# Kernel optimization log

Hardware: AMD Instinct MI355X
Metric: run time of the kernel (lower is better)

The kernel has to match this reference:

```python
import jax, jax.numpy as jnp
import numpy as np

B, NCLASS, NSUPP = 4096, 1000, 64
NCHUNK = NSUPP * NSUPP  # 4096, x's feature dim


def setup_inputs() -> dict:
    key = jax.random.key(0)
    k1, k2, k3 = jax.random.split(key, 3)
    x = jax.random.normal(k1, (B, NCHUNK), dtype=jnp.float32)
    # torch .uniform_(-1, 1)
    wSupp = jax.random.uniform(k2, (NCLASS, NSUPP), dtype=jnp.float32, minval=-1.0, maxval=1.0)
    chunk_map = jax.random.randint(k3, (NCLASS, NSUPP), 0, NCHUNK, dtype=jnp.int32)
    return {"x": x, "wSupp": wSupp, "chunk_map": chunk_map}


def reference(x, wSupp, chunk_map):
    # sparse_support: for each class i, feat_i = sum_j x[:, chunk_map[i,j]] * wSupp[i,j]; out = exp(feat)
    gathered = x[:, chunk_map]                      # [B, nClass, nSupp] gather via index map
    feats = jnp.einsum('bcs,cs->bc', gathered, wSupp)  # weighted sum over support
    return jnp.exp(feats)                           # [B, nClass]
```

## Files before the change

### kernel.cpp

```cpp
#include <hip/hip_runtime.h>
#include <hip/hip_fp16.h>


constexpr int B_       = 4096;
constexpr int NCLASS_  = 1000;
constexpr int NSUPP_   = 64;
constexpr int NCHUNK_  = 4096;
constexpr int BT       = 8;
constexpr int THREADS_ = 1024;
constexpr int SG_      = NSUPP_ / 4;
constexpr size_t CMT_BYTES = (size_t)SG_ * NCLASS_ * 16;
constexpr size_t WS_NEEDED = 2 * CMT_BYTES;

__global__ void transpose_cw_kernel(const int*   __restrict__ cm,
                                    const float* __restrict__ w,
                                    int4*        __restrict__ cmT,
                                    float4*      __restrict__ wT)
{
    const int tid = blockIdx.x * 256 + threadIdx.x;
    if (tid < SG_ * NCLASS_) {
        const int sg = tid / NCLASS_, c = tid % NCLASS_;
        cmT[tid] = reinterpret_cast<const int4*>(cm)[c * SG_ + sg];
    } else if (tid < 2 * SG_ * NCLASS_) {
        const int k = tid - SG_ * NCLASS_;
        const int sg = k / NCLASS_, c = k % NCLASS_;
        wT[k] = reinterpret_cast<const float4*>(w)[c * SG_ + sg];
    }
}

template <bool USET>
__global__ __launch_bounds__(THREADS_, 8)
void supp_gather_kernel(const float* __restrict__ x,
                        const float* __restrict__ wSupp,
                        const int*   __restrict__ cmap,
                        const float4* __restrict__ wT,
                        const int4*   __restrict__ cmT,
                        float*       __restrict__ out)
{
    __shared__ __align__(16) __half2 tile[NCHUNK_ * (BT / 2)];

    const int t  = threadIdx.x;
    const int rb = blockIdx.x * BT;

    #pragma unroll
    for (int p = 0; p < NCHUNK_ / THREADS_; ++p) {
        const int c = t + THREADS_ * p;
        float v[BT];
        #pragma unroll
        for (int bi = 0; bi < BT; ++bi)
            v[bi] = x[(size_t)(rb + bi) * NCHUNK_ + c];
        __half2 h[BT / 2];
        #pragma unroll
        for (int k = 0; k < BT / 2; ++k)
            h[k] = __floats2half2_rn(v[2 * k], v[2 * k + 1]);
        *reinterpret_cast<float4*>(&tile[(size_t)c * 4]) =
            *reinterpret_cast<float4*>(h);
    }
    __syncthreads();

    if (t < NCLASS_) {
        const int c = t;
        const float4* tile4 = reinterpret_cast<const float4*>(tile);
        float acc[BT] = {0.f, 0.f, 0.f, 0.f, 0.f, 0.f, 0.f, 0.f};

        int4   ci;
        float4 wf;
        if constexpr (USET) { ci = cmT[c];               wf = wT[c]; }
        else {
            ci = reinterpret_cast<const int4*>(cmap + c * NSUPP_)[0];
            wf = reinterpret_cast<const float4*>(wSupp + c * NSUPP_)[0];
        }

        for (int sg = 0; sg < SG_; ++sg) {
            float4 d0 = tile4[ci.x];
            float4 d1 = tile4[ci.y];
            float4 d2 = tile4[ci.z];
            float4 d3 = tile4[ci.w];
            const float4 wv = wf;

            const int sgn = (sg + 1 < SG_) ? sg + 1 : SG_ - 1;
            if constexpr (USET) {
                ci = cmT[sgn * NCLASS_ + c];
                wf = wT [sgn * NCLASS_ + c];
            } else {
                ci = reinterpret_cast<const int4*>(cmap + c * NSUPP_)[sgn];
                wf = reinterpret_cast<const float4*>(wSupp + c * NSUPP_)[sgn];
            }

            const float4* dp[4] = {&d0, &d1, &d2, &d3};
            const float   ws4[4] = {wv.x, wv.y, wv.z, wv.w};
            #pragma unroll
            for (int j = 0; j < 4; ++j) {
                const __half2* h2 = reinterpret_cast<const __half2*>(dp[j]);
                #pragma unroll
                for (int k = 0; k < 4; ++k) {
                    const float2 f = __half22float2(h2[k]);
                    acc[2 * k]     = fmaf(f.x, ws4[j], acc[2 * k]);
                    acc[2 * k + 1] = fmaf(f.y, ws4[j], acc[2 * k + 1]);
                }
            }
        }
        #pragma unroll
        for (int bi = 0; bi < BT; ++bi)
            out[(size_t)(rb + bi) * NCLASS_ + c] = __expf(acc[bi]);
    }
}

extern "C" void kernel_launch(void* const* d_in, const int* in_sizes, int n_in,
                              void* d_out, int out_size, void* d_ws, size_t ws_size,
                              hipStream_t stream) {
    const float* x  = (const float*)d_in[0];
    const float* w  = (const float*)d_in[1];
    const int*   cm = (const int*)d_in[2];
    float*       o  = (float*)d_out;

    int4*   cmT = (int4*)d_ws;
    float4* wT  = (float4*)((char*)d_ws + CMT_BYTES);

    if (ws_size >= WS_NEEDED) {
        const int total = 2 * SG_ * NCLASS_;
        transpose_cw_kernel<<<dim3((total + 255) / 256), dim3(256), 0, stream>>>(
            cm, w, cmT, wT);
        supp_gather_kernel<true><<<dim3(B_ / BT), dim3(THREADS_), 0, stream>>>(
            x, w, cm, wT, cmT, o);
    } else {
        supp_gather_kernel<false><<<dim3(B_ / BT), dim3(THREADS_), 0, stream>>>(
            x, w, cm, wT, cmT, o);
    }
}
```

Baseline: 117.8 us.

## Process two row tiles per block with double-buffered LDS prefetch

Each block now handles two 8-row tiles, using two LDS buffers. The global loads of the second tile's x rows are issued into registers before the first tile's gather-FMA loop, then converted and stored after it, so the load latency overlaps with compute. This doubles LDS per block to 64KB, halves the grid to 256 blocks, and raises register pressure from the 32 prefetched floats, which may reduce occupancy.

```diff
diff --git a/kernel.cpp b/kernel.cpp
--- a/kernel.cpp
+++ b/kernel.cpp
@@ -7,7 +7,9 @@
 constexpr int NSUPP_   = 64;
 constexpr int NCHUNK_  = 4096;
 constexpr int BT       = 8;
+constexpr int TILES_   = 2;
 constexpr int THREADS_ = 1024;
+constexpr int PCOLS_   = NCHUNK_ / THREADS_;
 constexpr int SG_      = NSUPP_ / 4;
 constexpr size_t CMT_BYTES = (size_t)SG_ * NCLASS_ * 16;
 constexpr size_t WS_NEEDED = 2 * CMT_BYTES;
@@ -29,7 +31,7 @@
 }
 
 template <bool USET>
-__global__ __launch_bounds__(THREADS_, 8)
+__global__ __launch_bounds__(THREADS_, 4)
 void supp_gather_kernel(const float* __restrict__ x,
                         const float* __restrict__ wSupp,
                         const int*   __restrict__ cmap,
@@ -37,13 +39,13 @@
                         const int4*   __restrict__ cmT,
                         float*       __restrict__ out)
 {
-    __shared__ __align__(16) __half2 tile[NCHUNK_ * (BT / 2)];
+    __shared__ __align__(16) __half2 buf[2][NCHUNK_ * (BT / 2)];
 
     const int t  = threadIdx.x;
-    const int rb = blockIdx.x * BT;
+    const int rb = blockIdx.x * (BT * TILES_);
 
     #pragma unroll
-    for (int p = 0; p < NCHUNK_ / THREADS_; ++p) {
+    for (int p = 0; p < PCOLS_; ++p) {
         const int c = t + THREADS_ * p;
         float v[BT];
         #pragma unroll
@@ -53,56 +55,86 @@
         #pragma unroll
         for (int k = 0; k < BT / 2; ++k)
             h[k] = __floats2half2_rn(v[2 * k], v[2 * k + 1]);
-        *reinterpret_cast<float4*>(&tile[(size_t)c * 4]) =
+        *reinterpret_cast<float4*>(&buf[0][(size_t)c * 4]) =
             *reinterpret_cast<float4*>(h);
     }
     __syncthreads();
 
-    if (t < NCLASS_) {
-        const int c = t;
-        const float4* tile4 = reinterpret_cast<const float4*>(tile);
-        float acc[BT] = {0.f, 0.f, 0.f, 0.f, 0.f, 0.f, 0.f, 0.f};
+    #pragma unroll
+    for (int tile = 0; tile < TILES_; ++tile) {
+        const int rbt = rb + tile * BT;
 
-        int4   ci;
-        float4 wf;
-        if constexpr (USET) { ci = cmT[c];               wf = wT[c]; }
-        else {
-            ci = reinterpret_cast<const int4*>(cmap + c * NSUPP_)[0];
-            wf = reinterpret_cast<const float4*>(wSupp + c * NSUPP_)[0];
+        float vn[PCOLS_][BT];
+        if (tile + 1 < TILES_) {
+            #pragma unroll
+            for (int p = 0; p < PCOLS_; ++p) {
+                const int c = t + THREADS_ * p;
+                #pragma unroll
+                for (int bi = 0; bi < BT; ++bi)
+                    vn[p][bi] = x[(size_t)(rbt + BT + bi) * NCHUNK_ + c];
+            }
         }
 
-        for (int sg = 0; sg < SG_; ++sg) {
-            float4 d0 = tile4[ci.x];
-            float4 d1 = tile4[ci.y];
-            float4 d2 = tile4[ci.z];
-            float4 d3 = tile4[ci.w];
-            const float4 wv = wf;
+        if (t < NCLASS_) {
+            const int c = t;
+            const float4* tile4 = reinterpret_cast<const float4*>(buf[tile]);
+            float acc[BT] = {0.f, 0.f, 0.f, 0.f, 0.f, 0.f, 0.f, 0.f};
 
-            const int sgn = (sg + 1 < SG_) ? sg + 1 : SG_ - 1;
-            if constexpr (USET) {
-                ci = cmT[sgn * NCLASS_ + c];
-                wf = wT [sgn * NCLASS_ + c];
-            } else {
-                ci = reinterpret_cast<const int4*>(cmap + c * NSUPP_)[sgn];
-                wf = reinterpret_cast<const float4*>(wSupp + c * NSUPP_)[sgn];
+            int4   ci;
+            float4 wf;
+            if constexpr (USET) { ci = cmT[c]; wf = wT[c]; }
+            else {
+                ci = reinterpret_cast<const int4*>(cmap + c * NSUPP_)[0];
+                wf = reinterpret_cast<const float4*>(wSupp + c * NSUPP_)[0];
             }
 
-            const float4* dp[4] = {&d0, &d1, &d2, &d3};
-            const float   ws4[4] = {wv.x, wv.y, wv.z, wv.w};
-            #pragma unroll
-            for (int j = 0; j < 4; ++j) {
-                const __half2* h2 = reinterpret_cast<const __half2*>(dp[j]);
+            for (int sg = 0; sg < SG_; ++sg) {
+                float4 d0 = tile4[ci.x];
+                float4 d1 = tile4[ci.y];
+                float4 d2 = tile4[ci.z];
+                float4 d3 = tile4[ci.w];
+                const float4 wv = wf;
+
+                const int sgn = (sg + 1 < SG_) ? sg + 1 : SG_ - 1;
+                if constexpr (USET) {
+                    ci = cmT[sgn * NCLASS_ + c];
+                    wf = wT [sgn * NCLASS_ + c];
+                } else {
+                    ci = reinterpret_cast<const int4*>(cmap + c * NSUPP_)[sgn];
+                    wf = reinterpret_cast<const float4*>(wSupp + c * NSUPP_)[sgn];
+                }
+
+                const float4* dp[4]  = {&d0, &d1, &d2, &d3};
+                const float   ws4[4] = {wv.x, wv.y, wv.z, wv.w};
                 #pragma unroll
-                for (int k = 0; k < 4; ++k) {
-                    const float2 f = __half22float2(h2[k]);
-                    acc[2 * k]     = fmaf(f.x, ws4[j], acc[2 * k]);
-                    acc[2 * k + 1] = fmaf(f.y, ws4[j], acc[2 * k + 1]);
+                for (int j = 0; j < 4; ++j) {
+                    const __half2* h2 = reinterpret_cast<const __half2*>(dp[j]);
+                    #pragma unroll
+                    for (int k = 0; k < 4; ++k) {
+                        const float2 f = __half22float2(h2[k]);
+                        acc[2 * k]     = fmaf(f.x, ws4[j], acc[2 * k]);
+                        acc[2 * k + 1] = fmaf(f.y, ws4[j], acc[2 * k + 1]);
+                    }
                 }
             }
+            #pragma unroll
+            for (int bi = 0; bi < BT; ++bi)
+                out[(size_t)(rbt + bi) * NCLASS_ + c] = __expf(acc[bi]);
         }
-        #pragma unroll
-        for (int bi = 0; bi < BT; ++bi)
-            out[(size_t)(rb + bi) * NCLASS_ + c] = __expf(acc[bi]);
+
+        if (tile + 1 < TILES_) {
+            #pragma unroll
+            for (int p = 0; p < PCOLS_; ++p) {
+                const int c = t + THREADS_ * p;
+                __half2 h[BT / 2];
+                #pragma unroll
+                for (int k = 0; k < BT / 2; ++k)
+                    h[k] = __floats2half2_rn(vn[p][2 * k], vn[p][2 * k + 1]);
+                *reinterpret_cast<float4*>(&buf[tile + 1][(size_t)c * 4]) =
+                    *reinterpret_cast<float4*>(h);
+            }
+            __syncthreads();
+        }
     }
 }
 
@@ -117,14 +149,15 @@
     int4*   cmT = (int4*)d_ws;
     float4* wT  = (float4*)((char*)d_ws + CMT_BYTES);
 
+    const dim3 grid(B_ / (BT * TILES_));
     if (ws_size >= WS_NEEDED) {
         const int total = 2 * SG_ * NCLASS_;
         transpose_cw_kernel<<<dim3((total + 255) / 256), dim3(256), 0, stream>>>(
             cm, w, cmT, wT);
-        supp_gather_kernel<true><<<dim3(B_ / BT), dim3(THREADS_), 0, stream>>>(
+        supp_gather_kernel<true><<<grid, dim3(THREADS_), 0, stream>>>(
             x, w, cm, wT, cmT, o);
     } else {
-        supp_gather_kernel<false><<<dim3(B_ / BT), dim3(THREADS_), 0, stream>>>(
+        supp_gather_kernel<false><<<grid, dim3(THREADS_), 0, stream>>>(
             x, w, cm, wT, cmT, o);
     }
 }
```

After: 116.6 us. About the same (-1.0%).

## Sort support indices by LDS bank residue and double-buffer index prefetch

Applied to the files above, without the earlier changes.

The preprocessing kernel now reorders each class's 64 support entries with a counting sort keyed on (index - class) mod 8. The intent is that lanes reading tile rows at the same step land in different shared-memory banks, reducing LDS bank conflicts in the gather. The main kernel also issues the first two index/weight groups before the x tile load and keeps a two-deep prefetch buffer with a fully unrolled loop. This adds a serial per-thread sort over only 1000 threads and increases register pressure from unrolling.

```diff
diff --git a/kernel.cpp b/kernel.cpp
--- a/kernel.cpp
+++ b/kernel.cpp
@@ -12,19 +12,37 @@
 constexpr size_t CMT_BYTES = (size_t)SG_ * NCLASS_ * 16;
 constexpr size_t WS_NEEDED = 2 * CMT_BYTES;
 
-__global__ void transpose_cw_kernel(const int*   __restrict__ cm,
-                                    const float* __restrict__ w,
-                                    int4*        __restrict__ cmT,
-                                    float4*      __restrict__ wT)
+__global__ void build_cw_kernel(const int*   __restrict__ cm,
+                                const float* __restrict__ w,
+                                int*         __restrict__ cmT,
+                                float*       __restrict__ wT)
 {
-    const int tid = blockIdx.x * 256 + threadIdx.x;
-    if (tid < SG_ * NCLASS_) {
-        const int sg = tid / NCLASS_, c = tid % NCLASS_;
-        cmT[tid] = reinterpret_cast<const int4*>(cm)[c * SG_ + sg];
-    } else if (tid < 2 * SG_ * NCLASS_) {
-        const int k = tid - SG_ * NCLASS_;
-        const int sg = k / NCLASS_, c = k % NCLASS_;
-        wT[k] = reinterpret_cast<const float4*>(w)[c * SG_ + sg];
+    const int c = blockIdx.x * 256 + threadIdx.x;
+    if (c >= NCLASS_) return;
+    const int*   ci = cm + c * NSUPP_;
+    const float* wi = w  + c * NSUPP_;
+
+    int cnt[8] = {0, 0, 0, 0, 0, 0, 0, 0};
+    int idxbuf[NSUPP_];
+    #pragma unroll 8
+    for (int s = 0; s < NSUPP_; ++s) {
+        const int v = ci[s];
+        idxbuf[s] = v;
+        ++cnt[(v - c) & 7];
+    }
+    int pos[8];
+    pos[0] = 0;
+    #pragma unroll
+    for (int r = 1; r < 8; ++r) pos[r] = pos[r - 1] + cnt[r - 1];
+
+    #pragma unroll 8
+    for (int s = 0; s < NSUPP_; ++s) {
+        const int v = idxbuf[s];
+        const int r = (v - c) & 7;
+        const int j = pos[r]++;
+        const int dst = ((j >> 2) * NCLASS_ + c) * 4 + (j & 3);
+        cmT[dst] = v;
+        wT [dst] = wi[s];
     }
 }
 
@@ -42,18 +60,32 @@
     const int t  = threadIdx.x;
     const int rb = blockIdx.x * BT;
 
+    int4   ci[2];
+    float4 wf[2];
+    if (t < NCLASS_) {
+        if constexpr (USET) {
+            ci[0] = cmT[0 * NCLASS_ + t];  wf[0] = wT[0 * NCLASS_ + t];
+            ci[1] = cmT[1 * NCLASS_ + t];  wf[1] = wT[1 * NCLASS_ + t];
+        } else {
+            ci[0] = reinterpret_cast<const int4*>(cmap + t * NSUPP_)[0];
+            wf[0] = reinterpret_cast<const float4*>(wSupp + t * NSUPP_)[0];
+            ci[1] = reinterpret_cast<const int4*>(cmap + t * NSUPP_)[1];
+            wf[1] = reinterpret_cast<const float4*>(wSupp + t * NSUPP_)[1];
+        }
+    }
+
     #pragma unroll
     for (int p = 0; p < NCHUNK_ / THREADS_; ++p) {
-        const int c = t + THREADS_ * p;
+        const int col = t + THREADS_ * p;
         float v[BT];
         #pragma unroll
         for (int bi = 0; bi < BT; ++bi)
-            v[bi] = x[(size_t)(rb + bi) * NCHUNK_ + c];
+            v[bi] = x[(size_t)(rb + bi) * NCHUNK_ + col];
         __half2 h[BT / 2];
         #pragma unroll
         for (int k = 0; k < BT / 2; ++k)
             h[k] = __floats2half2_rn(v[2 * k], v[2 * k + 1]);
-        *reinterpret_cast<float4*>(&tile[(size_t)c * 4]) =
+        *reinterpret_cast<float4*>(&tile[(size_t)col * 4]) =
             *reinterpret_cast<float4*>(h);
     }
     __syncthreads();
@@ -63,32 +95,29 @@
         const float4* tile4 = reinterpret_cast<const float4*>(tile);
         float acc[BT] = {0.f, 0.f, 0.f, 0.f, 0.f, 0.f, 0.f, 0.f};
 
-        int4   ci;
-        float4 wf;
-        if constexpr (USET) { ci = cmT[c];               wf = wT[c]; }
-        else {
-            ci = reinterpret_cast<const int4*>(cmap + c * NSUPP_)[0];
-            wf = reinterpret_cast<const float4*>(wSupp + c * NSUPP_)[0];
-        }
+        #pragma unroll
+        for (int sg = 0; sg < SG_; ++sg) {
+            const int cur = sg & 1;
+            const int4   cc = ci[cur];
+            const float4 ww = wf[cur];
 
-        for (int sg = 0; sg < SG_; ++sg) {
-            float4 d0 = tile4[ci.x];
-            float4 d1 = tile4[ci.y];
-            float4 d2 = tile4[ci.z];
-            float4 d3 = tile4[ci.w];
-            const float4 wv = wf;
+            float4 d0 = tile4[cc.x];
+            float4 d1 = tile4[cc.y];
+            float4 d2 = tile4[cc.z];
+            float4 d3 = tile4[cc.w];
 
-            const int sgn = (sg + 1 < SG_) ? sg + 1 : SG_ - 1;
-            if constexpr (USET) {
-                ci = cmT[sgn * NCLASS_ + c];
-                wf = wT [sgn * NCLASS_ + c];
-            } else {
-                ci = reinterpret_cast<const int4*>(cmap + c * NSUPP_)[sgn];
-                wf = reinterpret_cast<const float4*>(wSupp + c * NSUPP_)[sgn];
+            if (sg + 2 < SG_) {
+                if constexpr (USET) {
+                    ci[cur] = cmT[(sg + 2) * NCLASS_ + c];
+                    wf[cur] = wT [(sg + 2) * NCLASS_ + c];
+                } else {
+                    ci[cur] = reinterpret_cast<const int4*>(cmap + c * NSUPP_)[sg + 2];
+                    wf[cur] = reinterpret_cast<const float4*>(wSupp + c * NSUPP_)[sg + 2];
+                }
             }
 
-            const float4* dp[4] = {&d0, &d1, &d2, &d3};
-            const float   ws4[4] = {wv.x, wv.y, wv.z, wv.w};
+            const float4* dp[4]  = {&d0, &d1, &d2, &d3};
+            const float   ws4[4] = {ww.x, ww.y, ww.z, ww.w};
             #pragma unroll
             for (int j = 0; j < 4; ++j) {
                 const __half2* h2 = reinterpret_cast<const __half2*>(dp[j]);
@@ -114,17 +143,17 @@
     const int*   cm = (const int*)d_in[2];
     float*       o  = (float*)d_out;
 
-    int4*   cmT = (int4*)d_ws;
-    float4* wT  = (float4*)((char*)d_ws + CMT_BYTES);
+    int*   cmT = (int*)d_ws;
+    float* wT  = (float*)((char*)d_ws + CMT_BYTES);
 
+    const dim3 grid(B_ / BT);
     if (ws_size >= WS_NEEDED) {
-        const int total = 2 * SG_ * NCLASS_;
-        transpose_cw_kernel<<<dim3((total + 255) / 256), dim3(256), 0, stream>>>(
+        build_cw_kernel<<<dim3((NCLASS_ + 255) / 256), dim3(256), 0, stream>>>(
             cm, w, cmT, wT);
-        supp_gather_kernel<true><<<dim3(B_ / BT), dim3(THREADS_), 0, stream>>>(
-            x, w, cm, wT, cmT, o);
+        supp_gather_kernel<true><<<grid, dim3(THREADS_), 0, stream>>>(
+            x, w, cm, (const float4*)wT, (const int4*)cmT, o);
     } else {
-        supp_gather_kernel<false><<<dim3(B_ / BT), dim3(THREADS_), 0, stream>>>(
-            x, w, cm, wT, cmT, o);
+        supp_gather_kernel<false><<<grid, dim3(THREADS_), 0, stream>>>(
+            x, w, cm, (const float4*)wT, (const int4*)cmT, o);
     }
 }
```

Result: slower. 141.6 us (+20.2%).
